# Optimization experiments

Hardware: AMD Instinct MI355X
Metric: run time of the kernel (lower is better)

Reference implementation:

```python
import jax, jax.numpy as jnp
import numpy as np

B, S, D = 1, 2048, 2048
H, KVH, HD = 32, 8, 64  # head_dim = D // H
THETA = 10000.0
INIT_STD = 0.02


def _freqs_cos_sin(head_dim, end, theta):
    # precompute_freqs_cis, returned as (cos, sin) real tables [end, head_dim//2]
    freqs = 1.0 / theta ** (np.arange(0, head_dim, 2)[: head_dim // 2].astype(np.float32) / head_dim)
    t = np.arange(end)
    fr = np.outer(t, freqs).astype(np.float32)
    return jnp.asarray(np.cos(fr)), jnp.asarray(np.sin(fr))


def setup_inputs() -> dict:
    key = jax.random.key(0)
    ks = jax.random.split(key, 5)
    return {
        "hidden_states": jax.random.normal(ks[0], (B, S, D), jnp.float32),
        "wq": jax.random.normal(ks[1], (D, H * HD), jnp.float32) * INIT_STD,
        "wk": jax.random.normal(ks[2], (D, KVH * HD), jnp.float32) * INIT_STD,
        "wv": jax.random.normal(ks[3], (D, KVH * HD), jnp.float32) * INIT_STD,
        "wo": jax.random.normal(ks[4], (H * HD, D), jnp.float32) * INIT_STD,
        "position_ids": jnp.broadcast_to(jnp.arange(S, dtype=jnp.int32), (B, S)),
    }


def reference(hidden_states, wq, wk, wv, wo, position_ids):
    # QKV projections (no bias)
    xq = (hidden_states @ wq).reshape(B, S, H, HD)
    xk = (hidden_states @ wk).reshape(B, S, KVH, HD)
    xv = (hidden_states @ wv).reshape(B, S, KVH, HD)

    # rotary embedding: interleaved complex pairs over last dim
    cos_t, sin_t = _freqs_cos_sin(HD, S, THETA)        # [S, HD//2]
    cos = cos_t[position_ids][:, :, None, :]            # [B, S, 1, HD//2]
    sin = sin_t[position_ids][:, :, None, :]

    def rope(x):
        xr = x.astype(jnp.float32).reshape(*x.shape[:-1], -1, 2)
        a, b = xr[..., 0], xr[..., 1]
        # (a + i b) * (cos + i sin)
        ra = a * cos - b * sin
        rb = a * sin + b * cos
        return jnp.stack((ra, rb), axis=-1).reshape(x.shape)

    xq = rope(xq)
    xk = rope(xk)

    # GQA: repeat kv heads
    n_rep = H // KVH
    xk = jnp.repeat(xk[:, :, :, None, :], n_rep, axis=3).reshape(B, S, H, HD)
    xv = jnp.repeat(xv[:, :, :, None, :], n_rep, axis=3).reshape(B, S, H, HD)

    # causal masked softmax attention (full score matrix, as in dot_product_attention_weights)
    scores = jnp.einsum('bqhd,bkhd->bhqk', xq, xk) / np.float32(np.sqrt(HD))
    causal = jnp.tril(jnp.ones((S, S), dtype=bool))
    big_neg = jnp.finfo(jnp.float32).min
    scores = jnp.where(causal[None, None, :, :], scores, big_neg)
    attn = jax.nn.softmax(scores, axis=-1)

    out = jnp.einsum('bhqk,bkhd->bqhd', attn, xv).reshape(B, S, H * HD)
    return out @ wo
```

## Files before the change

### kernel.cpp

```cpp
#include <hip/hip_runtime.h>
#include <hip/hip_bf16.h>


using short8  = __attribute__((ext_vector_type(8))) short;
using f32x4   = __attribute__((ext_vector_type(4))) float;
using f32x16  = __attribute__((ext_vector_type(16))) float;
using f32x2   = __attribute__((ext_vector_type(2))) float;
using ushort4v= __attribute__((ext_vector_type(4))) unsigned short;

#define SEQ 2048
#define DIM 2048
#define NH  32
#define NKVH 8
#define HD  64
#define KVD 512
#define NQKV 3072

#define GLOAD_LDS16(g, l) \
  __builtin_amdgcn_global_load_lds((const __attribute__((address_space(1))) void*)(g), \
                                   (__attribute__((address_space(3))) void*)(l), 16, 0, 0)

__device__ __forceinline__ float bf2f(unsigned short u) {
  union { float f; unsigned v; } x; x.v = ((unsigned)u) << 16; return x.f;
}
__device__ __forceinline__ unsigned short f2bf(float f) {
  union { float f; unsigned v; } x; x.f = f;
  unsigned r = x.v + 0x7fffu + ((x.v >> 16) & 1u);
  return (unsigned short)(r >> 16);
}

__global__ __launch_bounds__(256) void k_cast(const float* __restrict__ src,
                                              unsigned short* __restrict__ dst, int n) {
  int idx = (blockIdx.x * 256 + threadIdx.x) * 4;
  if (idx < n) {
    f32x4 v = *(const f32x4*)(src + idx);
    ushort4v o;
    o[0] = f2bf(v[0]); o[1] = f2bf(v[1]); o[2] = f2bf(v[2]); o[3] = f2bf(v[3]);
    *(ushort4v*)(dst + idx) = o;
  }
}

__global__ __launch_bounds__(256) void k_tcast(const float* __restrict__ src, int C,
                                               unsigned short* __restrict__ dst) {
  __shared__ float tile[32][33];
  int c0 = blockIdx.x * 32, r0 = blockIdx.y * 32;
  int tx = threadIdx.x, ty = threadIdx.y;
  #pragma unroll
  for (int j = 0; j < 32; j += 8)
    tile[ty + j][tx] = src[(r0 + ty + j) * C + c0 + tx];
  __syncthreads();
  #pragma unroll
  for (int j = 0; j < 32; j += 8)
    dst[(c0 + ty + j) * 2048 + r0 + tx] = f2bf(tile[tx][ty + j]);
}

__global__ __launch_bounds__(256) void k_table(const int* __restrict__ pos,
                                               f32x2* __restrict__ tab) {
  int i = blockIdx.x * 256 + threadIdx.x;
  int s = i >> 5, p = i & 31;
  float freq = powf(10000.0f, -(float)(2 * p) / 64.0f);
  float ang = (float)pos[s] * freq;
  float sv, cv; sincosf(ang, &sv, &cv);
  f32x2 r; r[0] = cv; r[1] = sv;
  tab[i] = r;
}

template <int N, bool OUTF32>
__global__ __launch_bounds__(256) void k_gemm(const unsigned short* __restrict__ A,
                                              const unsigned short* __restrict__ Bt,
                                              void* __restrict__ Cout) {
  const int K = 2048;
  __shared__ unsigned short lA[128 * 64];
  __shared__ unsigned short lB[128 * 64];
  int m0 = blockIdx.y * 128, n0 = blockIdx.x * 128;
  int t = threadIdx.x, lane = t & 63, wid = t >> 6;
  int wr = wid >> 1, wc = wid & 1;
  int lr = lane & 15, lg = lane >> 4;

  f32x4 acc[4][4] = {};

  for (int k0 = 0; k0 < K; k0 += 64) {
    #pragma unroll
    for (int j = 0; j < 4; ++j) {
      int idx = t + 256 * j, row = idx >> 3, c8 = idx & 7;
      GLOAD_LDS16(A  + (m0 + row) * K + k0 + c8 * 8, lA + idx * 8);
      GLOAD_LDS16(Bt + (n0 + row) * K + k0 + c8 * 8, lB + idx * 8);
    }
    __syncthreads();
    #pragma unroll
    for (int kk = 0; kk < 64; kk += 32) {
      short8 af[4], bfr[4];
      #pragma unroll
      for (int i = 0; i < 4; ++i) {
        af[i]  = *(const short8*)(lA + (wr * 64 + i * 16 + lr) * 64 + kk + lg * 8);
        bfr[i] = *(const short8*)(lB + (wc * 64 + i * 16 + lr) * 64 + kk + lg * 8);
      }
      #pragma unroll
      for (int i = 0; i < 4; ++i)
        #pragma unroll
        for (int j = 0; j < 4; ++j)
          acc[i][j] = __builtin_amdgcn_mfma_f32_16x16x32_bf16(af[i], bfr[j], acc[i][j], 0, 0, 0);
    }
    __syncthreads();
  }
  #pragma unroll
  for (int i = 0; i < 4; ++i)
    #pragma unroll
    for (int j = 0; j < 4; ++j)
      #pragma unroll
      for (int r = 0; r < 4; ++r) {
        int row = m0 + wr * 64 + i * 16 + lg * 4 + r;
        int col = n0 + wc * 64 + j * 16 + lr;
        float v = acc[i][j][r];
        if constexpr (OUTF32) ((float*)Cout)[row * N + col] = v;
        else ((unsigned short*)Cout)[row * N + col] = f2bf(v);
      }
}

__global__ __launch_bounds__(256) void k_rope(const unsigned short* __restrict__ xqkv,
                                              const f32x2* __restrict__ tab,
                                              unsigned short* __restrict__ xq,
                                              unsigned short* __restrict__ xk) {
  int s = blockIdx.y;
  int j = blockIdx.x * 256 + threadIdx.x;
  bool isq = j < 1024;
  int col = isq ? (2 * j) : (DIM + 2 * (j - 1024));
  int p = (col >> 1) & 31;
  f32x2 cs = tab[s * 32 + p];
  unsigned both = *(const unsigned*)(xqkv + s * NQKV + col);
  float a = bf2f((unsigned short)(both & 0xffff));
  float b = bf2f((unsigned short)(both >> 16));
  float ra = a * cs[0] - b * cs[1];
  float rb = a * cs[1] + b * cs[0];
  const float QS = 0.125f * 1.44269504088896f;
  if (isq) { ra *= QS; rb *= QS; }
  unsigned pk = (unsigned)f2bf(ra) | ((unsigned)f2bf(rb) << 16);
  if (isq) *(unsigned*)(xq + s * DIM + col) = pk;
  else     *(unsigned*)(xk + s * KVD + (col - DIM)) = pk;
}

__global__ __launch_bounds__(256) void k_vt(const unsigned short* __restrict__ xqkv,
                                            unsigned short* __restrict__ xvT) {
  __shared__ unsigned short tile[32][33];
  int c0 = blockIdx.x * 32, s0 = blockIdx.y * 32;
  int tx = threadIdx.x, ty = threadIdx.y;
  #pragma unroll
  for (int j = 0; j < 32; j += 8)
    tile[ty + j][tx] = xqkv[(s0 + ty + j) * NQKV + 2560 + c0 + tx];
  __syncthreads();
  #pragma unroll
  for (int j = 0; j < 32; j += 8)
    xvT[(c0 + ty + j) * SEQ + s0 + tx] = tile[tx][ty + j];
}

__global__ __launch_bounds__(512) void k_attn(const unsigned short* __restrict__ xq,
                                              const unsigned short* __restrict__ xk,
                                              const unsigned short* __restrict__ xvT,
                                              unsigned short* __restrict__ attnout) {
  __shared__ float obuf[4][64 * 36];
  __shared__ float sm_m[4][2][32];
  __shared__ float sm_l[4][32];

  int wid = threadIdx.x >> 6, lane = threadIdx.x & 63;
  int kvh = blockIdx.x & 7, j = blockIdx.x >> 3;
  int h3 = wid & 3, half = wid >> 2;
  int h = kvh * 4 + h3;
  int lq = lane & 31, hi = lane >> 5;

  auto loadK = [&](int kv0, short8* d) {
    #pragma unroll
    for (int s = 0; s < 4; ++s)
      d[s] = *(const short8*)(xk + (kv0 + lq) * KVD + kvh * HD + s * 16 + hi * 8);
  };
  auto loadV = [&](int kv0, short8* d) {
    #pragma unroll
    for (int s2 = 0; s2 < 2; ++s2) {
      d[s2 * 2 + 0] = *(const short8*)(xvT + (kvh * HD + lq)      * SEQ + kv0 + s2 * 16 + hi * 8);
      d[s2 * 2 + 1] = *(const short8*)(xvT + (kvh * HD + 32 + lq) * SEQ + kv0 + s2 * 16 + hi * 8);
    }
  };

  #pragma unroll 1
  for (int ph = 0; ph < 2; ++ph) {
    int qb = ph ? (63 - j) : j;
    int q0 = qb * 32;
    int T = qb + 1;
    int c0 = (T + 1) >> 1;
    int t0 = half ? c0 : 0;
    int t1 = half ? T : c0;

    short8 qf[4];
    #pragma unroll
    for (int s = 0; s < 4; ++s)
      qf[s] = *(const short8*)(xq + (q0 + lq) * DIM + h * HD + s * 16 + hi * 8);

    f32x16 o0 = {}, o1 = {};
    float m = -3.0e38f, l = 0.0f;

    if (t0 < t1) {
      short8 kf[4], vf[4];
      loadK(t0 * 32, kf); loadV(t0 * 32, vf);

      for (int t = t0; t < t1; ++t) {
        int kv0 = t * 32;
        int kvn = min(t + 1, t1 - 1) * 32;
        short8 kn[4], vn[4];
        loadK(kvn, kn); loadV(kvn, vn);

        f32x16 st = {};
        __builtin_amdgcn_s_setprio(1);
        #pragma unroll
        for (int s = 0; s < 4; ++s)
          st = __builtin_amdgcn_mfma_f32_32x32x16_bf16(kf[s], qf[s], st, 0, 0, 0);
        __builtin_amdgcn_s_setprio(0);

        if (kv0 == q0) {
          #pragma unroll
          for (int r = 0; r < 16; ++r) {
            int kvl = (r & 3) + 8 * (r >> 2) + 4 * hi;
            if (kvl > lq) st[r] = -3.0e38f;
          }
        }
        float pmax = st[0];
        #pragma unroll
        for (int r = 1; r < 16; ++r) pmax = fmaxf(pmax, st[r]);
        pmax = fmaxf(pmax, __shfl_xor(pmax, 32));
        if (!__all(pmax - m <= 11.54f)) {
          float mnew = fmaxf(m, pmax);
          float scale = exp2f(m - mnew);
          #pragma unroll
          for (int r = 0; r < 16; ++r) {
            int ql = (r & 3) + 8 * (r >> 2) + 4 * hi;
            float sc = __shfl(scale, ql);
            o0[r] *= sc; o1[r] *= sc;
          }
          l *= scale;
          m = mnew;
        }
        float p[16], sum = 0.0f;
        #pragma unroll
        for (int r = 0; r < 16; ++r) { p[r] = exp2f(st[r] - m); sum += p[r]; }
        l += sum;
        unsigned w[8];
        #pragma unroll
        for (int i = 0; i < 8; ++i)
          asm("v_cvt_pk_bf16_f32 %0, %1, %2" : "=v"(w[i]) : "v"(p[2 * i]), "v"(p[2 * i + 1]));
        __builtin_amdgcn_s_setprio(1);
        #pragma unroll
        for (int s2 = 0; s2 < 2; ++s2) {
          int b = s2 * 4;
          unsigned sw0 = __shfl_xor(w[b + 0], 32);
          unsigned sw1 = __shfl_xor(w[b + 1], 32);
          unsigned sw2 = __shfl_xor(w[b + 2], 32);
          unsigned sw3 = __shfl_xor(w[b + 3], 32);
          union { unsigned u[4]; short8 s8; } pa;
          pa.u[0] = hi ? sw2 : w[b + 0];
          pa.u[1] = hi ? sw3 : w[b + 1];
          pa.u[2] = hi ? w[b + 2] : sw0;
          pa.u[3] = hi ? w[b + 3] : sw1;
          o0 = __builtin_amdgcn_mfma_f32_32x32x16_bf16(pa.s8, vf[s2 * 2 + 0], o0, 0, 0, 0);
          o1 = __builtin_amdgcn_mfma_f32_32x32x16_bf16(pa.s8, vf[s2 * 2 + 1], o1, 0, 0, 0);
        }
        __builtin_amdgcn_s_setprio(0);
        #pragma unroll
        for (int s = 0; s < 4; ++s) { kf[s] = kn[s]; vf[s] = vn[s]; }
      }
    }

    float lc = l + __shfl_xor(l, 32);
    if (hi == 0) sm_m[h3][half][lq] = m;
    __syncthreads();
    float mo = sm_m[h3][half ^ 1][lq];
    float mstar = fmaxf(m, mo);
    float s = exp2f(m - mstar);
    if (half) {
      if (hi == 0) sm_l[h3][lq] = lc * s;
      float* ob = &obuf[h3][lane * 36];
      #pragma unroll
      for (int r = 0; r < 16; ++r) {
        int ql = (r & 3) + 8 * (r >> 2) + 4 * hi;
        float sc = __shfl(s, ql);
        ob[r] = o0[r] * sc;
        ob[16 + r] = o1[r] * sc;
      }
    }
    __syncthreads();
    if (!half) {
      float lB = sm_l[h3][lq];
      float ltot = lc * s + lB;
      float linv = 1.0f / ltot;
      const float* ob = &obuf[h3][lane * 36];
      #pragma unroll
      for (int r = 0; r < 16; ++r) {
        int ql = (r & 3) + 8 * (r >> 2) + 4 * hi;
        float sc = __shfl(s, ql);
        float li = __shfl(linv, ql);
        int row = q0 + ql;
        attnout[row * DIM + h * HD + lq]      = f2bf((o0[r] * sc + ob[r]) * li);
        attnout[row * DIM + h * HD + 32 + lq] = f2bf((o1[r] * sc + ob[16 + r]) * li);
      }
    }
    if (ph == 0) __syncthreads();
  }
}

extern "C" void kernel_launch(void* const* d_in, const int* in_sizes, int n_in,
                              void* d_out, int out_size, void* d_ws, size_t ws_size,
                              hipStream_t stream) {
  const float* hs = (const float*)d_in[0];
  const float* wq = (const float*)d_in[1];
  const float* wk = (const float*)d_in[2];
  const float* wv = (const float*)d_in[3];
  const float* wo = (const float*)d_in[4];
  const int* pos  = (const int*)d_in[5];
  float* out = (float*)d_out;

  char* ws = (char*)d_ws;
  unsigned short* wqkvT = (unsigned short*)(ws);
  unsigned short* woT   = (unsigned short*)(ws + 12582912);
  unsigned short* hbf   = (unsigned short*)(ws + 20971520);
  unsigned short* xqkv  = (unsigned short*)(ws + 29360128);
  unsigned short* xq    = (unsigned short*)(ws + 41943040);
  unsigned short* xk    = (unsigned short*)(ws + 50331648);
  unsigned short* xvT   = (unsigned short*)(ws + 52428800);
  f32x2*          tab   = (f32x2*)(ws + 54525952);
  unsigned short* attnout = hbf;

  k_cast<<<4096, 256, 0, stream>>>(hs, hbf, SEQ * DIM);
  k_tcast<<<dim3(64, 64), dim3(32, 8), 0, stream>>>(wq, 2048, wqkvT);
  k_tcast<<<dim3(16, 64), dim3(32, 8), 0, stream>>>(wk, 512, wqkvT + 2048 * 2048);
  k_tcast<<<dim3(16, 64), dim3(32, 8), 0, stream>>>(wv, 512, wqkvT + 2560 * 2048);
  k_tcast<<<dim3(64, 64), dim3(32, 8), 0, stream>>>(wo, 2048, woT);
  k_table<<<256, 256, 0, stream>>>(pos, tab);

  k_gemm<NQKV, false><<<dim3(NQKV / 128, SEQ / 128), 256, 0, stream>>>(hbf, wqkvT, xqkv);

  k_rope<<<dim3(5, SEQ), 256, 0, stream>>>(xqkv, tab, xq, xk);
  k_vt<<<dim3(16, 64), dim3(32, 8), 0, stream>>>(xqkv, xvT);

  k_attn<<<256, 512, 0, stream>>>(xq, xk, xvT, attnout);

  k_gemm<DIM, true><<<dim3(DIM / 128, SEQ / 128), 256, 0, stream>>>(attnout, woT, out);
}
```

Baseline: 282.6 us.

## Stage K/V tiles in swizzled LDS and launch one block per query tile

```diff
diff --git a/kernel.cpp b/kernel.cpp
--- a/kernel.cpp
+++ b/kernel.cpp
@@ -153,154 +153,161 @@
     xvT[(c0 + ty + j) * SEQ + s0 + tx] = tile[tx][ty + j];
 }
 
-__global__ __launch_bounds__(512) void k_attn(const unsigned short* __restrict__ xq,
-                                              const unsigned short* __restrict__ xk,
-                                              const unsigned short* __restrict__ xvT,
-                                              unsigned short* __restrict__ attnout) {
-  __shared__ float obuf[4][64 * 36];
-  __shared__ float sm_m[4][2][32];
-  __shared__ float sm_l[4][32];
+__global__ __launch_bounds__(512, 4) void k_attn(const unsigned short* __restrict__ xq,
+                                                 const unsigned short* __restrict__ xk,
+                                                 const unsigned short* __restrict__ xvT,
+                                                 unsigned short* __restrict__ attnout) {
+  __shared__ __align__(16) char smem[38400];
 
   int wid = threadIdx.x >> 6, lane = threadIdx.x & 63;
-  int kvh = blockIdx.x & 7, j = blockIdx.x >> 3;
+  int kvh = blockIdx.x & 7, qb = 63 - (blockIdx.x >> 3);
   int h3 = wid & 3, half = wid >> 2;
   int h = kvh * 4 + h3;
   int lq = lane & 31, hi = lane >> 5;
-
-  auto loadK = [&](int kv0, short8* d) {
-    #pragma unroll
-    for (int s = 0; s < 4; ++s)
-      d[s] = *(const short8*)(xk + (kv0 + lq) * KVD + kvh * HD + s * 16 + hi * 8);
+  int q0 = qb * 32, T = qb + 1, c0 = (T + 1) >> 1;
+  int t0 = half ? c0 : 0, t1 = half ? T : c0, P = c0;
+
+  auto stageKV = [&](int tile, int buf) {
+    int kv0 = tile * 32;
+    int rl = lane >> 3;
+    const unsigned short* ks = xk + (kv0 + h3 * 8 + rl) * KVD + kvh * HD
+                                  + (((lane & 7) ^ rl) << 3);
+    GLOAD_LDS16(ks, smem + half * 8192 + buf * 4096 + h3 * 1024 + lane * 16);
+    int dl = lane >> 2;
+    const unsigned short* vs = xvT + (kvh * HD + h3 * 16 + dl) * SEQ + kv0
+                                   + (((lane & 3) ^ (dl & 3)) << 3);
+    GLOAD_LDS16(vs, smem + 16384 + half * 8192 + buf * 4096 + h3 * 1024 + lane * 16);
   };
-  auto loadV = [&](int kv0, short8* d) {
-    #pragma unroll
-    for (int s2 = 0; s2 < 2; ++s2) {
-      d[s2 * 2 + 0] = *(const short8*)(xvT + (kvh * HD + lq)      * SEQ + kv0 + s2 * 16 + hi * 8);
-      d[s2 * 2 + 1] = *(const short8*)(xvT + (kvh * HD + 32 + lq) * SEQ + kv0 + s2 * 16 + hi * 8);
-    }
-  };
-
-  #pragma unroll 1
-  for (int ph = 0; ph < 2; ++ph) {
-    int qb = ph ? (63 - j) : j;
-    int q0 = qb * 32;
-    int T = qb + 1;
-    int c0 = (T + 1) >> 1;
-    int t0 = half ? c0 : 0;
-    int t1 = half ? T : c0;
-
-    short8 qf[4];
-    #pragma unroll
-    for (int s = 0; s < 4; ++s)
-      qf[s] = *(const short8*)(xq + (q0 + lq) * DIM + h * HD + s * 16 + hi * 8);
-
-    f32x16 o0 = {}, o1 = {};
-    float m = -3.0e38f, l = 0.0f;
-
-    if (t0 < t1) {
+
+  short8 qf[4];
+  #pragma unroll
+  for (int s = 0; s < 4; ++s)
+    qf[s] = *(const short8*)(xq + (q0 + lq) * DIM + h * HD + s * 16 + hi * 8);
+
+  f32x16 o0 = {}, o1 = {};
+  float m = -3.0e38f, l = 0.0f;
+
+  stageKV(t0 < t1 ? t0 : 0, 0);
+  __syncthreads();
+  int cur = 0;
+
+  for (int i = 0; i < P; ++i) {
+    int t = t0 + i;
+    if (i + 1 < P) {
+      int tt = t0 + i + 1;
+      int tmax = (t1 > t0) ? (t1 - 1) : 0;
+      if (tt > tmax) tt = tmax;
+      stageKV(tt, cur ^ 1);
+    }
+    if (t < t1) {
+      int kv0 = t * 32;
+      const char* Kb = smem + half * 8192 + cur * 4096;
+      const char* Vb = smem + 16384 + half * 8192 + cur * 4096;
       short8 kf[4], vf[4];
-      loadK(t0 * 32, kf); loadV(t0 * 32, vf);
-
-      for (int t = t0; t < t1; ++t) {
-        int kv0 = t * 32;
-        int kvn = min(t + 1, t1 - 1) * 32;
-        short8 kn[4], vn[4];
-        loadK(kvn, kn); loadV(kvn, vn);
-
-        f32x16 st = {};
-        __builtin_amdgcn_s_setprio(1);
+      #pragma unroll
+      for (int s = 0; s < 4; ++s)
+        kf[s] = *(const short8*)(Kb + lq * 128 + ((s * 32 + hi * 16) ^ ((lq & 7) << 4)));
+      vf[0] = *(const short8*)(Vb + lq * 64        + ((hi * 16)      ^ ((lq & 3) << 4)));
+      vf[1] = *(const short8*)(Vb + (32 + lq) * 64 + ((hi * 16)      ^ ((lq & 3) << 4)));
+      vf[2] = *(const short8*)(Vb + lq * 64        + ((32 + hi * 16) ^ ((lq & 3) << 4)));
+      vf[3] = *(const short8*)(Vb + (32 + lq) * 64 + ((32 + hi * 16) ^ ((lq & 3) << 4)));
+
+      f32x16 st = {};
+      __builtin_amdgcn_s_setprio(1);
+      #pragma unroll
+      for (int s = 0; s < 4; ++s)
+        st = __builtin_amdgcn_mfma_f32_32x32x16_bf16(kf[s], qf[s], st, 0, 0, 0);
+      __builtin_amdgcn_s_setprio(0);
+
+      if (kv0 == q0) {
         #pragma unroll
-        for (int s = 0; s < 4; ++s)
-          st = __builtin_amdgcn_mfma_f32_32x32x16_bf16(kf[s], qf[s], st, 0, 0, 0);
-        __builtin_amdgcn_s_setprio(0);
-
-        if (kv0 == q0) {
-          #pragma unroll
-          for (int r = 0; r < 16; ++r) {
-            int kvl = (r & 3) + 8 * (r >> 2) + 4 * hi;
-            if (kvl > lq) st[r] = -3.0e38f;
-          }
+        for (int r = 0; r < 16; ++r) {
+          int kvl = (r & 3) + 8 * (r >> 2) + 4 * hi;
+          if (kvl > lq) st[r] = -3.0e38f;
         }
-        float pmax = st[0];
+      }
+      float pmax = st[0];
+      #pragma unroll
+      for (int r = 1; r < 16; ++r) pmax = fmaxf(pmax, st[r]);
+      pmax = fmaxf(pmax, __shfl_xor(pmax, 32));
+      if (!__all(pmax - m <= 11.54f)) {
+        float mnew = fmaxf(m, pmax);
+        float scale = exp2f(m - mnew);
         #pragma unroll
-        for (int r = 1; r < 16; ++r) pmax = fmaxf(pmax, st[r]);
-        pmax = fmaxf(pmax, __shfl_xor(pmax, 32));
-        if (!__all(pmax - m <= 11.54f)) {
-          float mnew = fmaxf(m, pmax);
-          float scale = exp2f(m - mnew);
-          #pragma unroll
-          for (int r = 0; r < 16; ++r) {
-            int ql = (r & 3) + 8 * (r >> 2) + 4 * hi;
-            float sc = __shfl(scale, ql);
-            o0[r] *= sc; o1[r] *= sc;
-          }
-          l *= scale;
-          m = mnew;
+        for (int r = 0; r < 16; ++r) {
+          int ql = (r & 3) + 8 * (r >> 2) + 4 * hi;
+          float sc = __shfl(scale, ql);
+          o0[r] *= sc; o1[r] *= sc;
         }
-        float p[16], sum = 0.0f;
-        #pragma unroll
-        for (int r = 0; r < 16; ++r) { p[r] = exp2f(st[r] - m); sum += p[r]; }
-        l += sum;
-        unsigned w[8];
-        #pragma unroll
-        for (int i = 0; i < 8; ++i)
-          asm("v_cvt_pk_bf16_f32 %0, %1, %2" : "=v"(w[i]) : "v"(p[2 * i]), "v"(p[2 * i + 1]));
-        __builtin_amdgcn_s_setprio(1);
-        #pragma unroll
-        for (int s2 = 0; s2 < 2; ++s2) {
-          int b = s2 * 4;
-          unsigned sw0 = __shfl_xor(w[b + 0], 32);
-          unsigned sw1 = __shfl_xor(w[b + 1], 32);
-          unsigned sw2 = __shfl_xor(w[b + 2], 32);
-          unsigned sw3 = __shfl_xor(w[b + 3], 32);
-          union { unsigned u[4]; short8 s8; } pa;
-          pa.u[0] = hi ? sw2 : w[b + 0];
-          pa.u[1] = hi ? sw3 : w[b + 1];
-          pa.u[2] = hi ? w[b + 2] : sw0;
-          pa.u[3] = hi ? w[b + 3] : sw1;
-          o0 = __builtin_amdgcn_mfma_f32_32x32x16_bf16(pa.s8, vf[s2 * 2 + 0], o0, 0, 0, 0);
-          o1 = __builtin_amdgcn_mfma_f32_32x32x16_bf16(pa.s8, vf[s2 * 2 + 1], o1, 0, 0, 0);
-        }
-        __builtin_amdgcn_s_setprio(0);
-        #pragma unroll
-        for (int s = 0; s < 4; ++s) { kf[s] = kn[s]; vf[s] = vn[s]; }
-      }
-    }
-
-    float lc = l + __shfl_xor(l, 32);
-    if (hi == 0) sm_m[h3][half][lq] = m;
+        l *= scale;
+        m = mnew;
+      }
+      float p[16], sum = 0.0f;
+      #pragma unroll
+      for (int r = 0; r < 16; ++r) { p[r] = exp2f(st[r] - m); sum += p[r]; }
+      l += sum;
+      unsigned w[8];
+      #pragma unroll
+      for (int i2 = 0; i2 < 8; ++i2)
+        asm("v_cvt_pk_bf16_f32 %0, %1, %2" : "=v"(w[i2]) : "v"(p[2 * i2]), "v"(p[2 * i2 + 1]));
+      __builtin_amdgcn_s_setprio(1);
+      #pragma unroll
+      for (int s2 = 0; s2 < 2; ++s2) {
+        int b = s2 * 4;
+        unsigned sw0 = __shfl_xor(w[b + 0], 32);
+        unsigned sw1 = __shfl_xor(w[b + 1], 32);
+        unsigned sw2 = __shfl_xor(w[b + 2], 32);
+        unsigned sw3 = __shfl_xor(w[b + 3], 32);
+        union { unsigned u[4]; short8 s8; } pa;
+        pa.u[0] = hi ? sw2 : w[b + 0];
+        pa.u[1] = hi ? sw3 : w[b + 1];
+        pa.u[2] = hi ? w[b + 2] : sw0;
+        pa.u[3] = hi ? w[b + 3] : sw1;
+        o0 = __builtin_amdgcn_mfma_f32_32x32x16_bf16(pa.s8, vf[s2 * 2 + 0], o0, 0, 0, 0);
+        o1 = __builtin_amdgcn_mfma_f32_32x32x16_bf16(pa.s8, vf[s2 * 2 + 1], o1, 0, 0, 0);
+      }
+      __builtin_amdgcn_s_setprio(0);
+    }
     __syncthreads();
-    float mo = sm_m[h3][half ^ 1][lq];
-    float mstar = fmaxf(m, mo);
-    float s = exp2f(m - mstar);
-    if (half) {
-      if (hi == 0) sm_l[h3][lq] = lc * s;
-      float* ob = &obuf[h3][lane * 36];
-      #pragma unroll
-      for (int r = 0; r < 16; ++r) {
-        int ql = (r & 3) + 8 * (r >> 2) + 4 * hi;
-        float sc = __shfl(s, ql);
-        ob[r] = o0[r] * sc;
-        ob[16 + r] = o1[r] * sc;
-      }
-    }
-    __syncthreads();
-    if (!half) {
-      float lB = sm_l[h3][lq];
-      float ltot = lc * s + lB;
-      float linv = 1.0f / ltot;
-      const float* ob = &obuf[h3][lane * 36];
-      #pragma unroll
-      for (int r = 0; r < 16; ++r) {
-        int ql = (r & 3) + 8 * (r >> 2) + 4 * hi;
-        float sc = __shfl(s, ql);
-        float li = __shfl(linv, ql);
-        int row = q0 + ql;
-        attnout[row * DIM + h * HD + lq]      = f2bf((o0[r] * sc + ob[r]) * li);
-        attnout[row * DIM + h * HD + 32 + lq] = f2bf((o1[r] * sc + ob[16 + r]) * li);
-      }
-    }
-    if (ph == 0) __syncthreads();
+    cur ^= 1;
+  }
+
+  float* obufp = (float*)smem;
+  float* smm   = (float*)(smem + 36864);
+  float* sml   = (float*)(smem + 37888);
+
+  float lc = l + __shfl_xor(l, 32);
+  if (hi == 0) smm[h3 * 64 + half * 32 + lq] = m;
+  __syncthreads();
+  float mo = smm[h3 * 64 + (half ^ 1) * 32 + lq];
+  float mstar = fmaxf(m, mo);
+  float s = exp2f(m - mstar);
+  if (half) {
+    if (hi == 0) sml[h3 * 32 + lq] = lc * s;
+    float* ob = obufp + h3 * 2304 + lane * 36;
+    #pragma unroll
+    for (int r = 0; r < 16; ++r) {
+      int ql = (r & 3) + 8 * (r >> 2) + 4 * hi;
+      float sc = __shfl(s, ql);
+      ob[r] = o0[r] * sc;
+      ob[16 + r] = o1[r] * sc;
+    }
+  }
+  __syncthreads();
+  if (!half) {
+    float lB = sml[h3 * 32 + lq];
+    float ltot = lc * s + lB;
+    float linv = 1.0f / ltot;
+    const float* ob = obufp + h3 * 2304 + lane * 36;
+    #pragma unroll
+    for (int r = 0; r < 16; ++r) {
+      int ql = (r & 3) + 8 * (r >> 2) + 4 * hi;
+      float sc = __shfl(s, ql);
+      float li = __shfl(linv, ql);
+      int row = q0 + ql;
+      attnout[row * DIM + h * HD + lq]      = f2bf((o0[r] * sc + ob[r]) * li);
+      attnout[row * DIM + h * HD + 32 + lq] = f2bf((o1[r] * sc + ob[16 + r]) * li);
+    }
   }
 }
 
@@ -338,7 +345,7 @@
   k_rope<<<dim3(5, SEQ), 256, 0, stream>>>(xqkv, tab, xq, xk);
   k_vt<<<dim3(16, 64), dim3(32, 8), 0, stream>>>(xqkv, xvT);
 
-  k_attn<<<256, 512, 0, stream>>>(xq, xk, xvT, attnout);
+  k_attn<<<512, 512, 0, stream>>>(xq, xk, xvT, attnout);
 
   k_gemm<DIM, true><<<dim3(DIM / 128, SEQ / 128), 256, 0, stream>>>(attnout, woT, out);
 }
```

New measurement: 264.3 us. -6.5%, faster.
